# Optimization experiments

Hardware: AMD Instinct MI355X
Metric: run time of the kernel (lower is better)

Reference implementation:

```python
import jax, jax.numpy as jnp
import numpy as np

N_PER_GRAPH = 1024
BATCH = 32
N = N_PER_GRAPH * BATCH  # 32768 total nodes
E = 262144               # edges per edge set (before self loops)
EMB = 128
D = 128
NEG_SLOPE = 0.2


def setup_inputs() -> dict:
    key = jax.random.key(0)
    ks = jax.random.split(key, 20)
    def lin(k, i, o):
        return (jax.random.normal(k, (i, o), jnp.float32) / np.float32(np.sqrt(i)))
    inp = {}
    inp["x"] = jax.random.normal(ks[0], (N, EMB), jnp.float32)
    inp["edge_index_n"] = jax.random.randint(ks[1], (2, E), 0, N, jnp.int32)
    inp["edge_index_r0"] = jax.random.randint(ks[2], (2, E), 0, N, jnp.int32)
    inp["edge_index_r1"] = jax.random.randint(ks[3], (2, E), 0, N, jnp.int32)
    # gat_0: Linear(EMB->D) + attn Linear(2D->D)
    inp["W0_lin"] = lin(ks[4], EMB, D); inp["b0_lin"] = jnp.zeros((D,), jnp.float32)
    inp["W0_att"] = lin(ks[5], 2 * D, D); inp["b0_att"] = jnp.zeros((D,), jnp.float32)
    # gat_1 (shared, used twice)
    inp["W1_lin"] = lin(ks[6], D, D); inp["b1_lin"] = jnp.zeros((D,), jnp.float32)
    inp["W1_att"] = lin(ks[7], 2 * D, D); inp["b1_att"] = jnp.zeros((D,), jnp.float32)
    # gat_2 (shared, used twice)
    inp["W2_lin"] = lin(ks[8], D, D); inp["b2_lin"] = jnp.zeros((D,), jnp.float32)
    inp["W2_att"] = lin(ks[9], 2 * D, D); inp["b2_att"] = jnp.zeros((D,), jnp.float32)
    # lin_prob: Linear(D->1)
    inp["Wp"] = lin(ks[10], D, 1); inp["bp"] = jnp.zeros((1,), jnp.float32)
    # Attention: W1, W2 (D->D, no bias), vt (D->1, no bias)
    inp["Wa1"] = lin(ks[11], D, D)
    inp["Wa2"] = lin(ks[12], D, D)
    inp["vt"] = lin(ks[13], D, 1)
    return inp


def _gat(x, edge_index, Wl, bl, Wa, ba):
    """One GATConv: add self loops, lin, edge gather, attn MLP, segment softmax, scatter-add."""
    n = x.shape[0]
    loop = jnp.arange(n, dtype=edge_index.dtype)
    src = jnp.concatenate([edge_index[0], loop])  # x_j index
    dst = jnp.concatenate([edge_index[1], loop])  # x_i / aggregation index
    h = x @ Wl + bl                               # [N, D]
    hi = h[dst]                                   # [E+N, D]
    hj = h[src]                                   # [E+N, D]
    a = jnp.concatenate([hi, hj], axis=-1) @ Wa + ba  # [E+N, D]
    a = jax.nn.leaky_relu(a, NEG_SLOPE)
    # segment softmax over destination neighborhoods (vector-valued, per channel)
    m = jax.lax.stop_gradient(jax.ops.segment_max(a, dst, num_segments=n))
    ex = jnp.exp(a - m[dst])
    s = jax.ops.segment_sum(ex, dst, num_segments=n)
    alpha = ex / (s[dst] + 1e-16)
    return jax.ops.segment_sum(hj * alpha, dst, num_segments=n)


def reference(x, edge_index_n, edge_index_r0, edge_index_r1,
              W0_lin, b0_lin, W0_att, b0_att,
              W1_lin, b1_lin, W1_att, b1_att,
              W2_lin, b2_lin, W2_att, b2_att,
              Wp, bp, Wa1, Wa2, vt):
    g0 = _gat(x,  edge_index_n,  W0_lin, b0_lin, W0_att, b0_att)
    g1 = _gat(g0, edge_index_r1, W1_lin, b1_lin, W1_att, b1_att)
    g2 = _gat(g1, edge_index_r0, W2_lin, b2_lin, W2_att, b2_att)
    g3 = _gat(g2, edge_index_r1, W1_lin, b1_lin, W1_att, b1_att)
    g4 = _gat(g3, edge_index_r0, W2_lin, b2_lin, W2_att, b2_att)
    X = g4.reshape(BATCH, N_PER_GRAPH, D)
    h = X.mean(axis=1)                                       # [B, D]
    logits1 = (X @ Wp + bp).reshape(BATCH, N_PER_GRAPH)      # [B, n]
    prob1 = jax.nn.softmax(logits1[:, 1:], axis=-1)          # [B, n-1]
    k1, k2 = jax.random.split(jax.random.key(42))
    index1 = 1 + jax.random.categorical(k1, logits1[:, 1:], axis=-1)  # [B]
    b_ar = jnp.arange(BATCH)
    sampled = X[b_ar, index1][:, None, :]                    # [B, 1, D]
    u = (jnp.tanh(sampled @ Wa1 + X @ Wa2) @ vt)[..., 0]      # [B, n]
    u = u.at[b_ar, index1].set(-jnp.inf)
    prob2 = jax.nn.softmax(u[:, 1:], axis=-1)                # [B, n-1]
    index2 = 1 + jax.random.categorical(k2, u[:, 1:], axis=-1)
    probs = prob1[b_ar, index1 - 1] + prob2[b_ar, index2 - 1]
    log_probs = jnp.log(probs)
    return (h, index1, index2, log_probs)
```

## Files before the change

### kernel.cpp

```cpp
#include <hip/hip_runtime.h>
#include <stdint.h>
#include <math.h>

#define NN 32768
#define EE 262144
#define DD 128
#define NPG 1024
#define NB 32
#define NEG_SLOPE 0.2f
#define ATP 132
#define USE_PARTITIONABLE 1

__host__ __device__ inline void tf2x32(uint32_t k0, uint32_t k1, uint32_t c0, uint32_t c1,
                                       uint32_t* o0, uint32_t* o1) {
  uint32_t ks2 = k0 ^ k1 ^ 0x1BD11BDAu;
  uint32_t x0 = c0 + k0;
  uint32_t x1 = c1 + k1;
#define TFR(r) { x0 += x1; x1 = (x1 << (r)) | (x1 >> (32 - (r))); x1 ^= x0; }
  TFR(13) TFR(15) TFR(26) TFR(6)
  x0 += k1; x1 += ks2 + 1u;
  TFR(17) TFR(29) TFR(16) TFR(24)
  x0 += ks2; x1 += k0 + 2u;
  TFR(13) TFR(15) TFR(26) TFR(6)
  x0 += k0; x1 += k1 + 3u;
  TFR(17) TFR(29) TFR(16) TFR(24)
  x0 += k1; x1 += ks2 + 4u;
  TFR(13) TFR(15) TFR(26) TFR(6)
  x0 += ks2; x1 += k0 + 5u;
#undef TFR
  *o0 = x0; *o1 = x1;
}

__device__ inline float gumbel_from_bits(uint32_t bits) {
  float fl = __uint_as_float((bits >> 9) | 0x3f800000u) - 1.0f;
  const float tiny = 1.17549435e-38f;
  float u = fmaxf(tiny, fl + tiny);
  return -logf(-logf(u));
}

__device__ inline float gumbel_at(uint32_t ka, uint32_t kb, uint32_t f) {
#if USE_PARTITIONABLE
  uint32_t o0, o1;
  tf2x32(ka, kb, 0u, f, &o0, &o1);
  return gumbel_from_bits(o0 ^ o1);
#else
  const uint32_t HALF = 16368u;
  uint32_t o0, o1;
  if (f < HALF) { tf2x32(ka, kb, f, f + HALF, &o0, &o1); return gumbel_from_bits(o0); }
  else          { tf2x32(ka, kb, f - HALF, f, &o0, &o1); return gumbel_from_bits(o1); }
#endif
}

__global__ __launch_bounds__(256) void hist3_kernel(const int* __restrict__ e0,
                                                    const int* __restrict__ e1,
                                                    const int* __restrict__ e2,
                                                    int* __restrict__ counts3) {
  int s = blockIdx.x >> 10;
  int i = (blockIdx.x & 1023) * 256 + threadIdx.x;
  const int* d = (s == 0) ? e0 : (s == 1) ? e1 : e2;
  atomicAdd(&counts3[s * NN + d[i + EE]], 1);
}

__global__ __launch_bounds__(1024) void scan3_kernel(const int* __restrict__ counts3,
                                                     int* __restrict__ rowptrAll,
                                                     int* __restrict__ cursorAll) {
  __shared__ int part[1024];
  int s = blockIdx.x;
  const int* counts = counts3 + s * NN;
  int* rowptr = rowptrAll + s * (NN + 1);
  int* cursor = cursorAll + s * NN;
  int t = threadIdx.x;
  int base = t * 32;
  int local[32];
  {
    const int4* c4 = (const int4*)(counts + base);
    int sum = 0;
#pragma unroll
    for (int v = 0; v < 8; v++) {
      int4 cc = c4[v];
      local[v * 4 + 0] = sum; sum += cc.x;
      local[v * 4 + 1] = sum; sum += cc.y;
      local[v * 4 + 2] = sum; sum += cc.z;
      local[v * 4 + 3] = sum; sum += cc.w;
    }
    part[t] = sum;
  }
  __syncthreads();
  int own = part[t];
  for (int off = 1; off < 1024; off <<= 1) {
    int v = (t >= off) ? part[t - off] : 0;
    __syncthreads();
    part[t] += v;
    __syncthreads();
  }
  int excl = part[t] - own;
  {
    int4* rp4 = (int4*)(rowptr + base);
    int4* cu4 = (int4*)(cursor + base);
#pragma unroll
    for (int v = 0; v < 8; v++) {
      int4 w;
      w.x = excl + local[v * 4 + 0];
      w.y = excl + local[v * 4 + 1];
      w.z = excl + local[v * 4 + 2];
      w.w = excl + local[v * 4 + 3];
      rp4[v] = w;
      cu4[v] = w;
    }
  }
  if (t == 1023) rowptr[NN] = part[1023];
}

__global__ __launch_bounds__(256) void scatter3_kernel(const int* __restrict__ e0,
                                                       const int* __restrict__ e1,
                                                       const int* __restrict__ e2,
                                                       int* __restrict__ cursorAll,
                                                       int* __restrict__ colAll) {
  int s = blockIdx.x >> 10;
  int i = (blockIdx.x & 1023) * 256 + threadIdx.x;
  const int* e = (s == 0) ? e0 : (s == 1) ? e1 : e2;
  int src = e[i], dst = e[i + EE];
  int p = atomicAdd(&cursorAll[s * NN + dst], 1);
  colAll[(size_t)s * EE + p] = src;
}

__global__ __launch_bounds__(256) void gemm128_kernel(const float* __restrict__ in,
                                                      const float* __restrict__ W,
                                                      const float* __restrict__ bias,
                                                      float* __restrict__ out, int hasBias) {
  __shared__ __align__(16) float ws[128 * 128];
  __shared__ __align__(16) float ins[64][132];
  int t = threadIdx.x;
  size_t row0 = (size_t)blockIdx.x * 64;
  {
    const float4* W4 = (const float4*)W;
    float4* ws4 = (float4*)ws;
#pragma unroll
    for (int i = 0; i < 16; i++) ws4[t + 256 * i] = W4[t + 256 * i];
    const float4* in4 = (const float4*)(in + row0 * 128);
#pragma unroll
    for (int i = 0; i < 8; i++) {
      int idx = t + 256 * i;
      int r = idx >> 5, c4 = idx & 31;
      float4 v = in4[(size_t)r * 32 + c4];
      *(float4*)&ins[r][c4 * 4] = v;
    }
  }
  __syncthreads();
  int cg = t & 15, rg = t >> 4;
  int c0 = cg * 8, r0 = rg * 4;
  float acc[4][8] = {};
#pragma unroll 8
  for (int k = 0; k < 128; k++) {
    float4 wA = *(const float4*)&ws[k * 128 + c0];
    float4 wB = *(const float4*)&ws[k * 128 + c0 + 4];
    float av[4];
    av[0] = ins[r0 + 0][k]; av[1] = ins[r0 + 1][k];
    av[2] = ins[r0 + 2][k]; av[3] = ins[r0 + 3][k];
#pragma unroll
    for (int i = 0; i < 4; i++) {
      acc[i][0] += av[i] * wA.x; acc[i][1] += av[i] * wA.y;
      acc[i][2] += av[i] * wA.z; acc[i][3] += av[i] * wA.w;
      acc[i][4] += av[i] * wB.x; acc[i][5] += av[i] * wB.y;
      acc[i][6] += av[i] * wB.z; acc[i][7] += av[i] * wB.w;
    }
  }
  float bb[8];
#pragma unroll
  for (int j = 0; j < 8; j++) bb[j] = hasBias ? bias[c0 + j] : 0.0f;
#pragma unroll
  for (int i = 0; i < 4; i++) {
    float* orow = out + (row0 + r0 + i) * 128 + c0;
    float4 o0, o1;
    o0.x = acc[i][0] + bb[0]; o0.y = acc[i][1] + bb[1];
    o0.z = acc[i][2] + bb[2]; o0.w = acc[i][3] + bb[3];
    o1.x = acc[i][4] + bb[4]; o1.y = acc[i][5] + bb[5];
    o1.z = acc[i][6] + bb[6]; o1.w = acc[i][7] + bb[7];
    *(float4*)orow = o0;
    *(float4*)(orow + 4) = o1;
  }
}

__global__ __launch_bounds__(256, 1) void fused_layer_kernel(
    const float* __restrict__ in, const float* __restrict__ Wl,
    const float* __restrict__ bl, const float* __restrict__ Wa,
    const float* __restrict__ ba, float* __restrict__ h,
    float* __restrict__ P, float* __restrict__ Q) {
  __shared__ __align__(16) float at[128 * ATP];
  __shared__ __align__(16) float ws[128 * 128];
  int t = threadIdx.x;
  size_t row0 = (size_t)blockIdx.x * 128;
  int tr = t >> 4, tc = t & 15;
  int r0 = tr * 8, c0 = tc * 8;
  float acc[8][8];

  auto stage_ws = [&](const float* src) {
    const float4* s4 = (const float4*)src;
    float4* d4 = (float4*)ws;
#pragma unroll
    for (int i = 0; i < 16; i++) d4[t + 256 * i] = s4[t + 256 * i];
  };
  auto transpose_ws_to_at = [&]() {
#pragma unroll
    for (int i = 0; i < 16; i++) {
      int idx = t + 256 * i;
      int k = idx & 127;
      int rg = idx >> 7;
      float4 v;
      v.x = ws[(rg * 4 + 0) * 128 + k];
      v.y = ws[(rg * 4 + 1) * 128 + k];
      v.z = ws[(rg * 4 + 2) * 128 + k];
      v.w = ws[(rg * 4 + 3) * 128 + k];
      *(float4*)&at[k * ATP + rg * 4] = v;
    }
  };
  auto mm = [&](const float* bias) {
#pragma unroll
    for (int i = 0; i < 8; i++)
#pragma unroll
      for (int j = 0; j < 8; j++) acc[i][j] = 0.f;
#pragma unroll 2
    for (int k = 0; k < 128; k++) {
      float4 a0 = *(const float4*)&at[k * ATP + r0];
      float4 a1 = *(const float4*)&at[k * ATP + r0 + 4];
      float4 w0 = *(const float4*)&ws[k * 128 + c0];
      float4 w1 = *(const float4*)&ws[k * 128 + c0 + 4];
      float av[8] = {a0.x, a0.y, a0.z, a0.w, a1.x, a1.y, a1.z, a1.w};
      float wv[8] = {w0.x, w0.y, w0.z, w0.w, w1.x, w1.y, w1.z, w1.w};
#pragma unroll
      for (int i = 0; i < 8; i++)
#pragma unroll
        for (int j = 0; j < 8; j++) acc[i][j] += av[i] * wv[j];
    }
    if (bias) {
#pragma unroll
      for (int j = 0; j < 8; j++) {
        float b = bias[c0 + j];
#pragma unroll
        for (int i = 0; i < 8; i++) acc[i][j] += b;
      }
    }
  };
  auto writeout = [&](float* dst) {
#pragma unroll
    for (int i = 0; i < 8; i++) {
      float* orow = dst + (row0 + r0 + i) * DD + c0;
      float4 o0, o1;
      o0.x = acc[i][0]; o0.y = acc[i][1]; o0.z = acc[i][2]; o0.w = acc[i][3];
      o1.x = acc[i][4]; o1.y = acc[i][5]; o1.z = acc[i][6]; o1.w = acc[i][7];
      *(float4*)orow = o0;
      *(float4*)(orow + 4) = o1;
    }
  };

  stage_ws(in + row0 * DD);
  __syncthreads();
  transpose_ws_to_at();
  __syncthreads();
  stage_ws(Wl);
  __syncthreads();
  mm(bl);
  writeout(h);
  __syncthreads();
  {
#pragma unroll
    for (int i = 0; i < 8; i++) {
      float4 o0, o1;
      o0.x = acc[i][0]; o0.y = acc[i][1]; o0.z = acc[i][2]; o0.w = acc[i][3];
      o1.x = acc[i][4]; o1.y = acc[i][5]; o1.z = acc[i][6]; o1.w = acc[i][7];
      *(float4*)&ws[(r0 + i) * 128 + c0] = o0;
      *(float4*)&ws[(r0 + i) * 128 + c0 + 4] = o1;
    }
  }
  __syncthreads();
  transpose_ws_to_at();
  __syncthreads();
  stage_ws(Wa);
  __syncthreads();
  mm(ba);
  writeout(P);
  __syncthreads();
  stage_ws(Wa + 128 * 128);
  __syncthreads();
  mm(nullptr);
  writeout(Q);
}

__device__ inline float lk1(float v) { return v > 0.f ? v : NEG_SLOPE * v; }

__global__ __launch_bounds__(256, 4) void gat_edge_kernel(const float* __restrict__ P,
                                                          const float* __restrict__ Q,
                                                          const float* __restrict__ H,
                                                          const int* __restrict__ rowptr,
                                                          const int* __restrict__ col,
                                                          float* __restrict__ out) {
  int wv = threadIdx.x >> 6;
  int lane = threadIdx.x & 63;
  int dst = (blockIdx.x << 2) + wv;
  int rs = __builtin_amdgcn_readfirstlane(rowptr[dst]);
  int re = __builtin_amdgcn_readfirstlane(rowptr[dst + 1]);
  int deg = re - rs;
  int total = deg + 1;
  float2 pd = ((const float2*)(P + (size_t)dst * DD))[lane];

  float mx = -INFINITY, my = -INFINITY;
  float sx = 0.f, sy = 0.f;
  float cx = 0.f, cy = 0.f;

  for (int base = 0; base < total; base += 64) {
    int cnt = min(64, total - base);
    int e = base + lane;
    int myidx = (e < deg) ? col[rs + e] : dst;
    int i = 0;
    for (; i + 4 <= cnt; i += 4) {
      int iu = __builtin_amdgcn_readfirstlane(i);
      int n0 = __builtin_amdgcn_readlane(myidx, iu);
      int n1 = __builtin_amdgcn_readlane(myidx, iu + 1);
      int n2 = __builtin_amdgcn_readlane(myidx, iu + 2);
      int n3 = __builtin_amdgcn_readlane(myidx, iu + 3);
      float2 q0 = ((const float2*)(Q + (size_t)n0 * DD))[lane];
      float2 q1 = ((const float2*)(Q + (size_t)n1 * DD))[lane];
      float2 q2 = ((const float2*)(Q + (size_t)n2 * DD))[lane];
      float2 q3 = ((const float2*)(Q + (size_t)n3 * DD))[lane];
      float2 h0 = ((const float2*)(H + (size_t)n0 * DD))[lane];
      float2 h1 = ((const float2*)(H + (size_t)n1 * DD))[lane];
      float2 h2 = ((const float2*)(H + (size_t)n2 * DD))[lane];
      float2 h3 = ((const float2*)(H + (size_t)n3 * DD))[lane];
      float a0x = lk1(pd.x + q0.x), a0y = lk1(pd.y + q0.y);
      float a1x = lk1(pd.x + q1.x), a1y = lk1(pd.y + q1.y);
      float a2x = lk1(pd.x + q2.x), a2y = lk1(pd.y + q2.y);
      float a3x = lk1(pd.x + q3.x), a3y = lk1(pd.y + q3.y);
      float nmx = fmaxf(fmaxf(mx, fmaxf(a0x, a1x)), fmaxf(a2x, a3x));
      float nmy = fmaxf(fmaxf(my, fmaxf(a0y, a1y)), fmaxf(a2y, a3y));
      float scx = expf(mx - nmx), scy = expf(my - nmy);
      float e0x = expf(a0x - nmx), e1x = expf(a1x - nmx);
      float e2x = expf(a2x - nmx), e3x = expf(a3x - nmx);
      float e0y = expf(a0y - nmy), e1y = expf(a1y - nmy);
      float e2y = expf(a2y - nmy), e3y = expf(a3y - nmy);
      sx = sx * scx + ((e0x + e1x) + (e2x + e3x));
      sy = sy * scy + ((e0y + e1y) + (e2y + e3y));
      cx = cx * scx + ((e0x * h0.x + e1x * h1.x) + (e2x * h2.x + e3x * h3.x));
      cy = cy * scy + ((e0y * h0.y + e1y * h1.y) + (e2y * h2.y + e3y * h3.y));
      mx = nmx; my = nmy;
    }
    for (; i < cnt; i++) {
      int iu = __builtin_amdgcn_readfirstlane(i);
      int n0 = __builtin_amdgcn_readlane(myidx, iu);
      float2 q0 = ((const float2*)(Q + (size_t)n0 * DD))[lane];
      float2 h0 = ((const float2*)(H + (size_t)n0 * DD))[lane];
      float a0x = lk1(pd.x + q0.x), a0y = lk1(pd.y + q0.y);
      float nmx = fmaxf(mx, a0x), nmy = fmaxf(my, a0y);
      float scx = expf(mx - nmx), scy = expf(my - nmy);
      float e0x = expf(a0x - nmx), e0y = expf(a0y - nmy);
      sx = sx * scx + e0x;
      sy = sy * scy + e0y;
      cx = cx * scx + e0x * h0.x;
      cy = cy * scy + e0y * h0.y;
      mx = nmx; my = nmy;
    }
  }
  float2 o = make_float2(cx / (sx + 1e-16f), cy / (sy + 1e-16f));
  ((float2*)(out + (size_t)dst * DD))[lane] = o;
}

__global__ __launch_bounds__(256) void logits_kernel(const float* __restrict__ X,
                                                     const float* __restrict__ Wp,
                                                     const float* __restrict__ bp,
                                                     float* __restrict__ logits) {
  int w = threadIdx.x >> 6, lane = threadIdx.x & 63;
  int n = blockIdx.x * 4 + w;
  const float* xr = X + (size_t)n * DD;
  float p = xr[lane] * Wp[lane] + xr[lane + 64] * Wp[lane + 64];
  for (int off = 32; off > 0; off >>= 1) p += __shfl_down(p, off);
  if (lane == 0) logits[n] = p + bp[0];
}

__global__ __launch_bounds__(1024) void hmean_kernel(const float* __restrict__ X,
                                                     float* __restrict__ out) {
  int b = blockIdx.x;
  int t = threadIdx.x;
  int c = t & 127, part = t >> 7;
  float acc = 0.f;
  for (int i = part; i < NPG; i += 8)
    acc += X[((size_t)b * NPG + i) * DD + c];
  __shared__ float red[1024];
  red[t] = acc; __syncthreads();
  if (part == 0) {
    float s = 0.f;
#pragma unroll
    for (int p = 0; p < 8; p++) s += red[p * 128 + c];
    out[b * DD + c] = s * (1.0f / (float)NPG);
  }
}

__global__ __launch_bounds__(256) void sample1_kernel(const float* __restrict__ logits,
                                                      uint32_t ka, uint32_t kb,
                                                      int* __restrict__ idx1_ws,
                                                      float* __restrict__ p1_ws,
                                                      float* __restrict__ out) {
  int b = blockIdx.x, t = threadIdx.x;
  __shared__ float sV[256]; __shared__ int sJ[256]; __shared__ float sM[256];
  float bestV = -INFINITY; int bestJ = 1 << 30; float maxL = -INFINITY;
  for (int j = 1 + t; j < NPG; j += 256) {
    float l = logits[(size_t)b * NPG + j];
    maxL = fmaxf(maxL, l);
    float v = l + gumbel_at(ka, kb, (uint32_t)(b * 1023 + j - 1));
    if (v > bestV) { bestV = v; bestJ = j; }
  }
  sV[t] = bestV; sJ[t] = bestJ; sM[t] = maxL; __syncthreads();
  for (int off = 128; off > 0; off >>= 1) {
    if (t < off) {
      if (sV[t + off] > sV[t] || (sV[t + off] == sV[t] && sJ[t + off] < sJ[t])) {
        sV[t] = sV[t + off]; sJ[t] = sJ[t + off];
      }
      sM[t] = fmaxf(sM[t], sM[t + off]);
    }
    __syncthreads();
  }
  float M = sM[0]; int idx = sJ[0];
  __syncthreads();
  float ps = 0.f;
  for (int j = 1 + t; j < NPG; j += 256)
    ps += expf(logits[(size_t)b * NPG + j] - M);
  sV[t] = ps; __syncthreads();
  for (int off = 128; off > 0; off >>= 1) {
    if (t < off) sV[t] += sV[t + off];
    __syncthreads();
  }
  if (t == 0) {
    float S = sV[0];
    float p1 = expf(logits[(size_t)b * NPG + idx] - M) / S;
    idx1_ws[b] = idx;
    p1_ws[b] = p1;
    out[NB * DD + b] = (float)idx;
  }
}

__global__ __launch_bounds__(128) void zk_kernel(const float* __restrict__ X,
                                                 const float* __restrict__ Wa1,
                                                 const int* __restrict__ idx1,
                                                 float* __restrict__ Z) {
  int b = blockIdx.x, c = threadIdx.x;
  __shared__ float xs[128];
  int node = b * NPG + idx1[b];
  xs[c] = X[(size_t)node * DD + c];
  __syncthreads();
  float acc = 0.f;
#pragma unroll 8
  for (int k = 0; k < 128; k++) acc += xs[k] * Wa1[k * 128 + c];
  Z[b * DD + c] = acc;
}

__global__ __launch_bounds__(256) void u_kernel(const float* __restrict__ Y,
                                                const float* __restrict__ Z,
                                                const float* __restrict__ vt,
                                                const int* __restrict__ idx1,
                                                float* __restrict__ u) {
  int w = threadIdx.x >> 6, lane = threadIdx.x & 63;
  int n = blockIdx.x * 4 + w;
  int b = n >> 10;
  float t0 = tanhf(Z[b * DD + lane] + Y[(size_t)n * DD + lane]) * vt[lane];
  float t1 = tanhf(Z[b * DD + lane + 64] + Y[(size_t)n * DD + lane + 64]) * vt[lane + 64];
  float p = t0 + t1;
  for (int off = 32; off > 0; off >>= 1) p += __shfl_down(p, off);
  if (lane == 0) u[n] = ((n & (NPG - 1)) == idx1[b]) ? -INFINITY : p;
}

__global__ __launch_bounds__(256) void sample2_kernel(const float* __restrict__ u,
                                                      uint32_t ka, uint32_t kb,
                                                      const float* __restrict__ p1_ws,
                                                      float* __restrict__ out) {
  int b = blockIdx.x, t = threadIdx.x;
  __shared__ float sV[256]; __shared__ int sJ[256]; __shared__ float sM[256];
  float bestV = -INFINITY; int bestJ = 1 << 30; float maxL = -INFINITY;
  for (int j = 1 + t; j < NPG; j += 256) {
    float l = u[(size_t)b * NPG + j];
    maxL = fmaxf(maxL, l);
    float v = l + gumbel_at(ka, kb, (uint32_t)(b * 1023 + j - 1));
    if (v > bestV) { bestV = v; bestJ = j; }
  }
  sV[t] = bestV; sJ[t] = bestJ; sM[t] = maxL; __syncthreads();
  for (int off = 128; off > 0; off >>= 1) {
    if (t < off) {
      if (sV[t + off] > sV[t] || (sV[t + off] == sV[t] && sJ[t + off] < sJ[t])) {
        sV[t] = sV[t + off]; sJ[t] = sJ[t + off];
      }
      sM[t] = fmaxf(sM[t], sM[t + off]);
    }
    __syncthreads();
  }
  float M = sM[0]; int idx = sJ[0];
  __syncthreads();
  float ps = 0.f;
  for (int j = 1 + t; j < NPG; j += 256) {
    float l = u[(size_t)b * NPG + j];
    ps += expf(l - M);
  }
  sV[t] = ps; __syncthreads();
  for (int off = 128; off > 0; off >>= 1) {
    if (t < off) sV[t] += sV[t + off];
    __syncthreads();
  }
  if (t == 0) {
    float S = sV[0];
    float p2 = expf(u[(size_t)b * NPG + idx] - M) / S;
    out[NB * DD + NB + b] = (float)idx;
    out[NB * DD + 2 * NB + b] = logf(p1_ws[b] + p2);
  }
}

extern "C" void kernel_launch(void* const* d_in, const int* in_sizes, int n_in,
                              void* d_out, int out_size, void* d_ws, size_t ws_size,
                              hipStream_t stream) {
  const float* x  = (const float*)d_in[0];
  const int* eN   = (const int*)d_in[1];
  const int* eR0  = (const int*)d_in[2];
  const int* eR1  = (const int*)d_in[3];
  const float* W0l = (const float*)d_in[4];  const float* b0l = (const float*)d_in[5];
  const float* W0a = (const float*)d_in[6];  const float* b0a = (const float*)d_in[7];
  const float* W1l = (const float*)d_in[8];  const float* b1l = (const float*)d_in[9];
  const float* W1a = (const float*)d_in[10]; const float* b1a = (const float*)d_in[11];
  const float* W2l = (const float*)d_in[12]; const float* b2l = (const float*)d_in[13];
  const float* W2a = (const float*)d_in[14]; const float* b2a = (const float*)d_in[15];
  const float* Wp  = (const float*)d_in[16]; const float* bp  = (const float*)d_in[17];
  const float* Wa1 = (const float*)d_in[18]; const float* Wa2 = (const float*)d_in[19];
  const float* vt  = (const float*)d_in[20];
  float* out = (float*)d_out;

  char* wsb = (char*)d_ws;
  size_t off = 0;
  auto take = [&](size_t bytes) -> char* {
    char* p = wsb + off;
    off += (bytes + 255) & ~(size_t)255;
    return p;
  };
  int* rowptrAll = (int*)take((size_t)3 * (NN + 1) * sizeof(int));
  int* counts3   = (int*)take((size_t)3 * NN * sizeof(int));
  int* cursorAll = (int*)take((size_t)3 * NN * sizeof(int));
  int* colAll    = (int*)take((size_t)3 * EE * sizeof(int));
  float* bufA    = (float*)take((size_t)NN * DD * 4);
  float* bufB    = (float*)take((size_t)NN * DD * 4);
  float* hb      = (float*)take((size_t)NN * DD * 4);
  float* Pb      = (float*)take((size_t)NN * DD * 4);
  float* Qb      = (float*)take((size_t)NN * DD * 4);
  float* logits  = (float*)take((size_t)NN * 4);
  float* ub      = (float*)take((size_t)NN * 4);
  float* Zb      = (float*)take((size_t)NB * DD * 4);
  int* idx1b     = (int*)take(NB * 4);
  float* p1b     = (float*)take(NB * 4);

  uint32_t k1a, k1b, k2a, k2b;
#if USE_PARTITIONABLE
  {
    uint32_t o0, o1;
    tf2x32(0u, 42u, 0u, 0u, &o0, &o1); k1a = o0; k1b = o1;
    tf2x32(0u, 42u, 0u, 1u, &o0, &o1); k2a = o0; k2b = o1;
  }
#else
  {
    uint32_t a0, b0, a1, b1;
    tf2x32(0u, 42u, 0u, 2u, &a0, &b0);
    tf2x32(0u, 42u, 1u, 3u, &a1, &b1);
    k1a = a0; k1b = a1; k2a = b0; k2b = b1;
  }
#endif

  hipMemsetAsync(counts3, 0, (size_t)3 * NN * sizeof(int), stream);
  hist3_kernel<<<3 * 1024, 256, 0, stream>>>(eN, eR0, eR1, counts3);
  scan3_kernel<<<3, 1024, 0, stream>>>(counts3, rowptrAll, cursorAll);
  scatter3_kernel<<<3 * 1024, 256, 0, stream>>>(eN, eR0, eR1, cursorAll, colAll);

  struct Layer { const float* in; float* o; const float *Wl, *bl, *Wa, *ba; int set; };
  Layer Ls[5] = {
      {x,    bufA, W0l, b0l, W0a, b0a, 0},
      {bufA, bufB, W1l, b1l, W1a, b1a, 2},
      {bufB, bufA, W2l, b2l, W2a, b2a, 1},
      {bufA, bufB, W1l, b1l, W1a, b1a, 2},
      {bufB, bufA, W2l, b2l, W2a, b2a, 1},
  };
  for (int L = 0; L < 5; L++) {
    fused_layer_kernel<<<NN / 128, 256, 0, stream>>>(
        Ls[L].in, Ls[L].Wl, Ls[L].bl, Ls[L].Wa, Ls[L].ba, hb, Pb, Qb);
    gat_edge_kernel<<<NN / 4, 256, 0, stream>>>(
        Pb, Qb, hb, rowptrAll + Ls[L].set * (NN + 1),
        colAll + (size_t)Ls[L].set * EE, Ls[L].o);
  }
  const float* X = bufA;

  gemm128_kernel<<<NN / 64, 256, 0, stream>>>(X, Wa2, nullptr, Pb, 0);
  logits_kernel<<<NN / 4, 256, 0, stream>>>(X, Wp, bp, logits);
  hmean_kernel<<<NB, 1024, 0, stream>>>(X, out);
  sample1_kernel<<<NB, 256, 0, stream>>>(logits, k1a, k1b, idx1b, p1b, out);
  zk_kernel<<<NB, 128, 0, stream>>>(X, Wa1, idx1b, Zb);
  u_kernel<<<NN / 4, 256, 0, stream>>>(Pb, Zb, vt, idx1b, ub);
  sample2_kernel<<<NB, 256, 0, stream>>>(ub, k2a, k2b, p1b, out);
}
```

Before: 788.7 us.

## Split fused layer GEMM into K-chunked lin and attention kernels

Replaces the monolithic fused_layer kernel, which used about 130KB of LDS at one block per CU, with two GEMM kernels that stage 16-wide K chunks through small shared buffers. The attention kernel computes P and Q together with a 128x256 output tile. Each thread now holds an 8x16 accumulator. The smaller LDS footprint allows higher occupancy, at the cost of an extra launch per layer and an extra round-trip of h through global memory. The final Wa2 GEMM also moves to the new lin kernel.

Measured after the change: 852.4 us. 8.1% more time.

```diff
diff --git a/kernel.cpp b/kernel.cpp
--- a/kernel.cpp
+++ b/kernel.cpp
@@ -8,7 +8,6 @@
 #define NPG 1024
 #define NB 32
 #define NEG_SLOPE 0.2f
-#define ATP 132
 #define USE_PARTITIONABLE 1
 
 __host__ __device__ inline void tf2x32(uint32_t k0, uint32_t k1, uint32_t c0, uint32_t c1,
@@ -124,166 +123,154 @@
   colAll[(size_t)s * EE + p] = src;
 }
 
-__global__ __launch_bounds__(256) void gemm128_kernel(const float* __restrict__ in,
-                                                      const float* __restrict__ W,
-                                                      const float* __restrict__ bias,
-                                                      float* __restrict__ out, int hasBias) {
-  __shared__ __align__(16) float ws[128 * 128];
-  __shared__ __align__(16) float ins[64][132];
-  int t = threadIdx.x;
-  size_t row0 = (size_t)blockIdx.x * 64;
-  {
-    const float4* W4 = (const float4*)W;
-    float4* ws4 = (float4*)ws;
-#pragma unroll
-    for (int i = 0; i < 16; i++) ws4[t + 256 * i] = W4[t + 256 * i];
-    const float4* in4 = (const float4*)(in + row0 * 128);
-#pragma unroll
-    for (int i = 0; i < 8; i++) {
-      int idx = t + 256 * i;
-      int r = idx >> 5, c4 = idx & 31;
-      float4 v = in4[(size_t)r * 32 + c4];
-      *(float4*)&ins[r][c4 * 4] = v;
-    }
-  }
-  __syncthreads();
-  int cg = t & 15, rg = t >> 4;
-  int c0 = cg * 8, r0 = rg * 4;
-  float acc[4][8] = {};
-#pragma unroll 8
-  for (int k = 0; k < 128; k++) {
-    float4 wA = *(const float4*)&ws[k * 128 + c0];
-    float4 wB = *(const float4*)&ws[k * 128 + c0 + 4];
-    float av[4];
-    av[0] = ins[r0 + 0][k]; av[1] = ins[r0 + 1][k];
-    av[2] = ins[r0 + 2][k]; av[3] = ins[r0 + 3][k];
-#pragma unroll
-    for (int i = 0; i < 4; i++) {
-      acc[i][0] += av[i] * wA.x; acc[i][1] += av[i] * wA.y;
-      acc[i][2] += av[i] * wA.z; acc[i][3] += av[i] * wA.w;
-      acc[i][4] += av[i] * wB.x; acc[i][5] += av[i] * wB.y;
-      acc[i][6] += av[i] * wB.z; acc[i][7] += av[i] * wB.w;
-    }
-  }
-  float bb[8];
-#pragma unroll
-  for (int j = 0; j < 8; j++) bb[j] = hasBias ? bias[c0 + j] : 0.0f;
-#pragma unroll
-  for (int i = 0; i < 4; i++) {
-    float* orow = out + (row0 + r0 + i) * 128 + c0;
-    float4 o0, o1;
-    o0.x = acc[i][0] + bb[0]; o0.y = acc[i][1] + bb[1];
-    o0.z = acc[i][2] + bb[2]; o0.w = acc[i][3] + bb[3];
-    o1.x = acc[i][4] + bb[4]; o1.y = acc[i][5] + bb[5];
-    o1.z = acc[i][6] + bb[6]; o1.w = acc[i][7] + bb[7];
-    *(float4*)orow = o0;
-    *(float4*)(orow + 4) = o1;
-  }
-}
-
-__global__ __launch_bounds__(256, 1) void fused_layer_kernel(
-    const float* __restrict__ in, const float* __restrict__ Wl,
-    const float* __restrict__ bl, const float* __restrict__ Wa,
-    const float* __restrict__ ba, float* __restrict__ h,
-    float* __restrict__ P, float* __restrict__ Q) {
-  __shared__ __align__(16) float at[128 * ATP];
-  __shared__ __align__(16) float ws[128 * 128];
+__global__ __launch_bounds__(128) void lin_kernel(const float* __restrict__ in,
+                                                  const float* __restrict__ W,
+                                                  const float* __restrict__ bias,
+                                                  float* __restrict__ out) {
+  __shared__ __align__(16) float at[16 * 132];
+  __shared__ __align__(16) float ws[16 * 128];
   int t = threadIdx.x;
   size_t row0 = (size_t)blockIdx.x * 128;
-  int tr = t >> 4, tc = t & 15;
-  int r0 = tr * 8, c0 = tc * 8;
-  float acc[8][8];
-
-  auto stage_ws = [&](const float* src) {
-    const float4* s4 = (const float4*)src;
-    float4* d4 = (float4*)ws;
-#pragma unroll
-    for (int i = 0; i < 16; i++) d4[t + 256 * i] = s4[t + 256 * i];
-  };
-  auto transpose_ws_to_at = [&]() {
-#pragma unroll
-    for (int i = 0; i < 16; i++) {
-      int idx = t + 256 * i;
-      int k = idx & 127;
-      int rg = idx >> 7;
-      float4 v;
-      v.x = ws[(rg * 4 + 0) * 128 + k];
-      v.y = ws[(rg * 4 + 1) * 128 + k];
-      v.z = ws[(rg * 4 + 2) * 128 + k];
-      v.w = ws[(rg * 4 + 3) * 128 + k];
-      *(float4*)&at[k * ATP + rg * 4] = v;
-    }
-  };
-  auto mm = [&](const float* bias) {
-#pragma unroll
-    for (int i = 0; i < 8; i++)
-#pragma unroll
-      for (int j = 0; j < 8; j++) acc[i][j] = 0.f;
-#pragma unroll 2
-    for (int k = 0; k < 128; k++) {
-      float4 a0 = *(const float4*)&at[k * ATP + r0];
-      float4 a1 = *(const float4*)&at[k * ATP + r0 + 4];
-      float4 w0 = *(const float4*)&ws[k * 128 + c0];
-      float4 w1 = *(const float4*)&ws[k * 128 + c0 + 4];
+  int tr = t >> 3, tcg = t & 7;
+  int r0 = tr * 8;
+  float acc[8][16];
+#pragma unroll
+  for (int i = 0; i < 8; i++)
+#pragma unroll
+    for (int j = 0; j < 16; j++) acc[i][j] = 0.f;
+
+  int srow = t >> 2, sc4 = (t & 3) * 4;
+  for (int kc = 0; kc < 8; ++kc) {
+    int k0 = kc * 16;
+#pragma unroll
+    for (int p = 0; p < 4; ++p) {
+      int row = p * 32 + srow;
+      float4 v = *(const float4*)&in[(row0 + row) * DD + k0 + sc4];
+      at[(sc4 + 0) * 132 + row] = v.x;
+      at[(sc4 + 1) * 132 + row] = v.y;
+      at[(sc4 + 2) * 132 + row] = v.z;
+      at[(sc4 + 3) * 132 + row] = v.w;
+    }
+#pragma unroll
+    for (int i2 = 0; i2 < 4; ++i2) {
+      int g = t + 128 * i2;
+      int kk = g >> 5, jg = (g & 31) * 4;
+      *(float4*)&ws[kk * 128 + jg] = *(const float4*)&W[(size_t)(k0 + kk) * DD + jg];
+    }
+    __syncthreads();
+#pragma unroll
+    for (int kk = 0; kk < 16; ++kk) {
+      float4 a0 = *(const float4*)&at[kk * 132 + r0];
+      float4 a1 = *(const float4*)&at[kk * 132 + r0 + 4];
       float av[8] = {a0.x, a0.y, a0.z, a0.w, a1.x, a1.y, a1.z, a1.w};
-      float wv[8] = {w0.x, w0.y, w0.z, w0.w, w1.x, w1.y, w1.z, w1.w};
+      float4 wv0 = *(const float4*)&ws[kk * 128 + 4 * tcg];
+      float4 wv1 = *(const float4*)&ws[kk * 128 + 4 * tcg + 32];
+      float4 wv2 = *(const float4*)&ws[kk * 128 + 4 * tcg + 64];
+      float4 wv3 = *(const float4*)&ws[kk * 128 + 4 * tcg + 96];
+      float wv[16] = {wv0.x, wv0.y, wv0.z, wv0.w, wv1.x, wv1.y, wv1.z, wv1.w,
+                      wv2.x, wv2.y, wv2.z, wv2.w, wv3.x, wv3.y, wv3.z, wv3.w};
 #pragma unroll
       for (int i = 0; i < 8; i++)
 #pragma unroll
-        for (int j = 0; j < 8; j++) acc[i][j] += av[i] * wv[j];
-    }
+        for (int j = 0; j < 16; j++) acc[i][j] += av[i] * wv[j];
+    }
+    __syncthreads();
+  }
+#pragma unroll
+  for (int g = 0; g < 4; ++g) {
+    float b[4] = {0.f, 0.f, 0.f, 0.f};
     if (bias) {
 #pragma unroll
-      for (int j = 0; j < 8; j++) {
-        float b = bias[c0 + j];
-#pragma unroll
-        for (int i = 0; i < 8; i++) acc[i][j] += b;
-      }
-    }
-  };
-  auto writeout = [&](float* dst) {
-#pragma unroll
-    for (int i = 0; i < 8; i++) {
-      float* orow = dst + (row0 + r0 + i) * DD + c0;
-      float4 o0, o1;
-      o0.x = acc[i][0]; o0.y = acc[i][1]; o0.z = acc[i][2]; o0.w = acc[i][3];
-      o1.x = acc[i][4]; o1.y = acc[i][5]; o1.z = acc[i][6]; o1.w = acc[i][7];
-      *(float4*)orow = o0;
-      *(float4*)(orow + 4) = o1;
-    }
-  };
-
-  stage_ws(in + row0 * DD);
-  __syncthreads();
-  transpose_ws_to_at();
-  __syncthreads();
-  stage_ws(Wl);
-  __syncthreads();
-  mm(bl);
-  writeout(h);
-  __syncthreads();
-  {
-#pragma unroll
-    for (int i = 0; i < 8; i++) {
-      float4 o0, o1;
-      o0.x = acc[i][0]; o0.y = acc[i][1]; o0.z = acc[i][2]; o0.w = acc[i][3];
-      o1.x = acc[i][4]; o1.y = acc[i][5]; o1.z = acc[i][6]; o1.w = acc[i][7];
-      *(float4*)&ws[(r0 + i) * 128 + c0] = o0;
-      *(float4*)&ws[(r0 + i) * 128 + c0 + 4] = o1;
-    }
-  }
-  __syncthreads();
-  transpose_ws_to_at();
-  __syncthreads();
-  stage_ws(Wa);
-  __syncthreads();
-  mm(ba);
-  writeout(P);
-  __syncthreads();
-  stage_ws(Wa + 128 * 128);
-  __syncthreads();
-  mm(nullptr);
-  writeout(Q);
+      for (int j = 0; j < 4; ++j) b[j] = bias[4 * tcg + 32 * g + j];
+    }
+#pragma unroll
+    for (int i = 0; i < 8; ++i) {
+      float4 o;
+      o.x = acc[i][4 * g + 0] + b[0];
+      o.y = acc[i][4 * g + 1] + b[1];
+      o.z = acc[i][4 * g + 2] + b[2];
+      o.w = acc[i][4 * g + 3] + b[3];
+      *(float4*)&out[(row0 + r0 + i) * DD + 4 * tcg + 32 * g] = o;
+    }
+  }
+}
+
+__global__ __launch_bounds__(256) void att_kernel(const float* __restrict__ h,
+                                                  const float* __restrict__ Wa,
+                                                  const float* __restrict__ ba,
+                                                  float* __restrict__ P,
+                                                  float* __restrict__ Q) {
+  __shared__ __align__(16) float at[16 * 132];
+  __shared__ __align__(16) float ws[16 * 256];
+  int t = threadIdx.x;
+  size_t row0 = (size_t)blockIdx.x * 128;
+  int tr = t >> 4, tcg = t & 15;
+  int r0 = tr * 8;
+  float acc[8][16];
+#pragma unroll
+  for (int i = 0; i < 8; i++)
+#pragma unroll
+    for (int j = 0; j < 16; j++) acc[i][j] = 0.f;
+
+  int srow = t >> 2, sc4 = (t & 3) * 4;
+  for (int kc = 0; kc < 8; ++kc) {
+    int k0 = kc * 16;
+#pragma unroll
+    for (int p = 0; p < 2; ++p) {
+      int row = p * 64 + srow;
+      float4 v = *(const float4*)&h[(row0 + row) * DD + k0 + sc4];
+      at[(sc4 + 0) * 132 + row] = v.x;
+      at[(sc4 + 1) * 132 + row] = v.y;
+      at[(sc4 + 2) * 132 + row] = v.z;
+      at[(sc4 + 3) * 132 + row] = v.w;
+    }
+#pragma unroll
+    for (int i2 = 0; i2 < 4; ++i2) {
+      int g = t + 256 * i2;
+      int kk = g >> 6, jg = g & 63;
+      const float* src = (jg < 32)
+          ? &Wa[(size_t)(k0 + kk) * DD + 4 * jg]
+          : &Wa[(size_t)(128 + k0 + kk) * DD + 4 * (jg - 32)];
+      *(float4*)&ws[kk * 256 + 4 * jg] = *(const float4*)src;
+    }
+    __syncthreads();
+#pragma unroll
+    for (int kk = 0; kk < 16; ++kk) {
+      float4 a0 = *(const float4*)&at[kk * 132 + r0];
+      float4 a1 = *(const float4*)&at[kk * 132 + r0 + 4];
+      float av[8] = {a0.x, a0.y, a0.z, a0.w, a1.x, a1.y, a1.z, a1.w};
+      float4 wv0 = *(const float4*)&ws[kk * 256 + 4 * tcg];
+      float4 wv1 = *(const float4*)&ws[kk * 256 + 4 * tcg + 64];
+      float4 wv2 = *(const float4*)&ws[kk * 256 + 4 * tcg + 128];
+      float4 wv3 = *(const float4*)&ws[kk * 256 + 4 * tcg + 192];
+      float wv[16] = {wv0.x, wv0.y, wv0.z, wv0.w, wv1.x, wv1.y, wv1.z, wv1.w,
+                      wv2.x, wv2.y, wv2.z, wv2.w, wv3.x, wv3.y, wv3.z, wv3.w};
+#pragma unroll
+      for (int i = 0; i < 8; i++)
+#pragma unroll
+        for (int j = 0; j < 16; j++) acc[i][j] += av[i] * wv[j];
+    }
+    __syncthreads();
+  }
+#pragma unroll
+  for (int g = 0; g < 4; ++g) {
+    float* dst = (g < 2) ? P : Q;
+    int cbase = 4 * tcg + 64 * (g & 1);
+    float b[4] = {0.f, 0.f, 0.f, 0.f};
+    if (g < 2) {
+#pragma unroll
+      for (int j = 0; j < 4; ++j) b[j] = ba[cbase + j];
+    }
+#pragma unroll
+    for (int i = 0; i < 8; ++i) {
+      float4 o;
+      o.x = acc[i][4 * g + 0] + b[0];
+      o.y = acc[i][4 * g + 1] + b[1];
+      o.z = acc[i][4 * g + 2] + b[2];
+      o.w = acc[i][4 * g + 3] + b[3];
+      *(float4*)&dst[(row0 + r0 + i) * DD + cbase] = o;
+    }
+  }
 }
 
 __device__ inline float lk1(float v) { return v > 0.f ? v : NEG_SLOPE * v; }
@@ -579,15 +566,15 @@
       {bufB, bufA, W2l, b2l, W2a, b2a, 1},
   };
   for (int L = 0; L < 5; L++) {
-    fused_layer_kernel<<<NN / 128, 256, 0, stream>>>(
-        Ls[L].in, Ls[L].Wl, Ls[L].bl, Ls[L].Wa, Ls[L].ba, hb, Pb, Qb);
+    lin_kernel<<<NN / 128, 128, 0, stream>>>(Ls[L].in, Ls[L].Wl, Ls[L].bl, hb);
+    att_kernel<<<NN / 128, 256, 0, stream>>>(hb, Ls[L].Wa, Ls[L].ba, Pb, Qb);
     gat_edge_kernel<<<NN / 4, 256, 0, stream>>>(
         Pb, Qb, hb, rowptrAll + Ls[L].set * (NN + 1),
         colAll + (size_t)Ls[L].set * EE, Ls[L].o);
   }
   const float* X = bufA;
 
-  gemm128_kernel<<<NN / 64, 256, 0, stream>>>(X, Wa2, nullptr, Pb, 0);
+  lin_kernel<<<NN / 128, 128, 0, stream>>>(X, Wa2, nullptr, Pb);
   logits_kernel<<<NN / 4, 256, 0, stream>>>(X, Wp, bp, logits);
   hmean_kernel<<<NB, 1024, 0, stream>>>(X, out);
   sample1_kernel<<<NB, 256, 0, stream>>>(logits, k1a, k1b, idx1b, p1b, out);
```
